# Kernel tuning notes

Measured on AMD Instinct MI355X. Metric: run time of the kernel, lower is better.

## Reference

```python
import jax, jax.numpy as jnp
import numpy as np

N = 48000      # total nodes
R = 16         # topological rounds
NPR = 3000     # nodes per round
DEG = 2        # children (incoming edges) per parent node
EPR = NPR * DEG
H = 128        # h_size
X = 128        # x_size
G = 16         # graphs in batch
PG = N // G    # nodes per graph == max_node_num


def setup_inputs() -> dict:
    key = jax.random.key(0)
    ks = jax.random.split(key, 8)
    j = np.arange(NPR)
    # round r parents are nodes [r*NPR,(r+1)*NPR); children come from round r-1
    edges = []
    for r in range(1, R):
        src = r * NPR + np.repeat(j, DEG)                                  # parent (edge_index[0])
        dst = (r - 1) * NPR + np.stack([j, (j + 1) % NPR], 1).ravel()       # child  (edge_index[1])
        edges.append(np.stack([src, dst], 0))
    edges_r = jnp.asarray(np.stack(edges, 0), dtype=jnp.int32)             # [R-1, 2, EPR]
    order_r = jnp.asarray(np.stack([r * NPR + j for r in range(1, R)], 0), dtype=jnp.int32)  # [R-1, NPR]
    order0 = jnp.asarray(j, dtype=jnp.int32)                               # leaves, round 0
    graph_idx = jnp.asarray(np.arange(N) // PG, dtype=jnp.int32)
    pos_idx = jnp.asarray(np.arange(N) % PG, dtype=jnp.int32)
    s = jnp.float32(0.05)
    return {
        'x': jax.random.normal(ks[0], (N, X), jnp.float32),
        'edge_labels_r': jax.random.randint(ks[1], (R - 1, EPR, 1), 0, 2).astype(jnp.float32),
        'W_iou': jax.random.normal(ks[2], (3 * H, X), jnp.float32) * s,
        'W_f': jax.random.normal(ks[3], (H, X), jnp.float32) * s,
        'b_iou': jax.random.normal(ks[4], (1, 3 * H), jnp.float32) * s,
        'b_f': jax.random.normal(ks[5], (1, H), jnp.float32) * s,
        'U_iou': jax.random.normal(ks[6], (3 * H, 2 * H), jnp.float32) * s,
        'U_f': jax.random.normal(ks[7], (H, 2 * H), jnp.float32) * s,
        'edges_r': edges_r,
        'order0': order0,
        'order_r': order_r,
        'graph_idx': graph_idx,
        'pos_idx': pos_idx,
        'graph_num': G,
        'max_node_num': PG,
    }


def reference(x, edge_labels_r, W_iou, W_f, b_iou, b_f, U_iou, U_f,
              edges_r, order0, order_r, graph_idx, pos_idx, graph_num, max_node_num):
    n = x.shape[0]
    h_size = W_f.shape[0]
    iou_x = x @ W_iou.T    # [n, 3h]
    wf_x = x @ W_f.T       # [n, h]

    def node_update(h, c, iou_mid, order):
        iou = iou_x[order] + iou_mid[order] + b_iou
        i, o, u = jnp.split(iou, 3, axis=1)
        c_temp = jax.nn.sigmoid(i) * jnp.tanh(u) + c[order]
        c = c.at[order].set(c_temp)
        h = h.at[order].set(jax.nn.sigmoid(o) * jnp.tanh(c_temp))
        return h, c

    h = jnp.zeros((n, h_size), x.dtype)
    c = jnp.zeros_like(h)
    iou_mid = jnp.zeros((n, 3 * h_size), x.dtype)
    h, c = node_update(h, c, iou_mid, order0)

    def step(carry, inp):
        h, c, iou_mid = carry
        edges, lab, order = inp        # edges [2,EPR], lab [EPR,1], order [NPR]
        src, child = edges[0], edges[1]
        h_j = h[child]
        # h_t0 (label==0 part) first, then h_t1, matching torch cat order
        h_two = jnp.concatenate([(1.0 - lab) * h_j, lab * h_j], axis=1)   # [EPR, 2h]
        iou_mid = iou_mid.at[src].add(h_two @ U_iou.T)
        f = jax.nn.sigmoid(wf_x[child] + h_two @ U_f.T + b_f)
        c = c.at[src].add(f * jnp.clip(c[child], -1e14, 1e14))
        h, c = node_update(h, c, iou_mid, order)
        return (h, c, iou_mid), None

    (h, c, iou_mid), _ = jax.lax.scan(step, (h, c, iou_mid), (edges_r, edge_labels_r, order_r))

    h_out = jnp.zeros((graph_num, max_node_num, h_size), x.dtype)
    return h_out.at[graph_idx, pos_idx].set(h)
```

## Files before the change

### kernel.cpp

```cpp
#include <hip/hip_runtime.h>
#include <math.h>

#define NN   48000
#define RR   16
#define NPR  3000
#define EPR  6000
#define HH   128
#define XX   128
#define C512 512

#define PPB  12
#define NB   250
#define MAXP 27
#define MAXE 52

typedef __attribute__((ext_vector_type(8))) short short8;
typedef __attribute__((ext_vector_type(8))) unsigned short ushort8;
typedef __attribute__((ext_vector_type(4))) float f32x4;

__device__ __forceinline__ float sigm(float v) {
  return __fdividef(1.0f, 1.0f + __expf(-v));
}
__device__ __forceinline__ float tanh_fast(float v) {
  return 1.0f - 2.0f * __fdividef(1.0f, 1.0f + __expf(2.0f * v));
}
__device__ __forceinline__ float clampc(float v) {
  return fminf(fmaxf(v, -1e14f), 1e14f);
}
__device__ __forceinline__ unsigned short f2bf(float f) {
  unsigned int u = __float_as_uint(f);
  unsigned int r = (u + 0x7FFFu + ((u >> 16) & 1u)) >> 16;
  return (unsigned short)r;
}

__global__ __launch_bounds__(256) void prep_wu(
    const float* __restrict__ Wiou, const float* __restrict__ Wf,
    const float* __restrict__ Uiou, const float* __restrict__ Uf,
    const float* __restrict__ b_iou, const float* __restrict__ b_f,
    unsigned short* __restrict__ Wbf, unsigned short* __restrict__ Ubf,
    float* __restrict__ biof) {
  int t = blockIdx.x * 256 + threadIdx.x;
  if (t < 512) biof[t] = (t < 384) ? b_iou[t] : b_f[t - 384];
  if (t < 512 * 128) {
    int r = t >> 7, c = t & 127;
    float v = (r < 384) ? Wiou[r * 128 + c] : Wf[(r - 384) * 128 + c];
    Wbf[t] = f2bf(v);
  }
  if (t < 512 * 256) {
    int r = t >> 8, c = t & 255;
    float v = (r < 384) ? Uiou[r * 256 + c] : Uf[(r - 384) * 256 + c];
    Ubf[t] = f2bf(v);
  }
}

__global__ __launch_bounds__(256) void pre_gemm_mfma(
    const float* __restrict__ x, const unsigned short* __restrict__ Wbf,
    const float* __restrict__ biof, float* __restrict__ pre) {
  __shared__ __align__(16) unsigned short A[128][136];
  const int n0 = blockIdx.x * 128;
  const int k0 = blockIdx.y * 128;
  const int t = threadIdx.x;

#pragma unroll
  for (int pass = 0; pass < 4; ++pass) {
    int row = (t >> 3) + pass * 32;
    int cb = (t & 7) * 16;
    const float* src = x + (size_t)(n0 + row) * XX + cb;
    unsigned short hv[16];
#pragma unroll
    for (int i = 0; i < 16; i += 4) {
      float4 v = *(const float4*)(src + i);
      hv[i] = f2bf(v.x); hv[i + 1] = f2bf(v.y);
      hv[i + 2] = f2bf(v.z); hv[i + 3] = f2bf(v.w);
    }
    *(ushort8*)&A[row][cb] = *(ushort8*)&hv[0];
    *(ushort8*)&A[row][cb + 8] = *(ushort8*)&hv[8];
  }
  __syncthreads();

  const int wave = t >> 6, lane = t & 63;
  const int wm = (wave & 1) * 64;
  const int wn = (wave >> 1) * 64;
  const int ln = lane & 15, q = lane >> 4;

  f32x4 acc[4][4];
#pragma unroll
  for (int mt = 0; mt < 4; ++mt)
#pragma unroll
    for (int nt = 0; nt < 4; ++nt)
      acc[mt][nt] = (f32x4){0.f, 0.f, 0.f, 0.f};

#pragma unroll
  for (int kt = 0; kt < 4; ++kt) {
    short8 af[4], bfr[4];
#pragma unroll
    for (int mt = 0; mt < 4; ++mt)
      af[mt] = *(const short8*)&A[wm + mt * 16 + ln][kt * 32 + q * 8];
#pragma unroll
    for (int nt = 0; nt < 4; ++nt)
      bfr[nt] = *(const short8*)(Wbf + (size_t)(k0 + wn + nt * 16 + ln) * 128 +
                                 kt * 32 + q * 8);
#pragma unroll
    for (int mt = 0; mt < 4; ++mt)
#pragma unroll
      for (int nt = 0; nt < 4; ++nt)
        acc[mt][nt] = __builtin_amdgcn_mfma_f32_16x16x32_bf16(
            af[mt], bfr[nt], acc[mt][nt], 0, 0, 0);
  }
  float bv[4];
#pragma unroll
  for (int nt = 0; nt < 4; ++nt) bv[nt] = biof[k0 + wn + nt * 16 + ln];
#pragma unroll
  for (int mt = 0; mt < 4; ++mt)
#pragma unroll
    for (int nt = 0; nt < 4; ++nt)
#pragma unroll
      for (int r = 0; r < 4; ++r)
        pre[(size_t)(n0 + wm + mt * 16 + q * 4 + r) * C512 +
            (k0 + wn + nt * 16 + ln)] = acc[mt][nt][r] + bv[nt];
}

__global__ __launch_bounds__(1024, 4) void rounds_halo(
    const float* __restrict__ pre, const unsigned short* __restrict__ Ubf,
    const float* __restrict__ labels, const int* __restrict__ order0,
    const int* __restrict__ order_r, float* __restrict__ hout) {
  __shared__ float Cp[2][MAXP + 1][132];
  __shared__ unsigned char labA[15 * 56];
  __shared__ int ordA[16 * 28];
  __shared__ __align__(16) unsigned short Abuf[56][264];
  __shared__ float Sb[26][392];
  __shared__ float Fb[52][132];

  const int t = threadIdx.x;
  const int b = blockIdx.x;
  const int g0 = b * PPB;
  const int w = t >> 6, lane = t & 63;
  const int ln = lane & 15, q = lane >> 4;

  if (t < 15 * 56) {
    int rr = t / 56, e = t - rr * 56;
    int p = e >> 1;
    int gp = g0 + p; if (gp >= NPR) gp -= NPR;
    labA[t] = (labels[(size_t)rr * EPR + 2 * gp + (e & 1)] >= 0.5f) ? 1 : 0;
  }
  if (t < 16 * 28) {
    int rr = t / 28, p = t - rr * 28;
    int gp = g0 + p; if (gp >= NPR) gp -= NPR;
    ordA[t] = (rr == 0) ? order0[gp] : order_r[(size_t)(rr - 1) * NPR + gp];
  }
  __syncthreads();

  const unsigned short* const ubase = Ubf + (size_t)(w * 32 + ln) * 256 + q * 8;

#pragma unroll
  for (int i = 0; i < 4; ++i) {
    int idx = t + i * 1024;
    int row = idx >> 7, j = idx & 127;
    if (row < MAXP) {
      int n = ordA[row];
      const float* pr = pre + (size_t)n * C512;
      float ct = sigm(pr[j]) * tanh_fast(pr[256 + j]);
      float ht = sigm(pr[128 + j]) * tanh_fast(ct);
      Cp[0][row][j] = ct;
      unsigned short hb = f2bf(ht);
      int L0 = labA[2 * row];
      Abuf[2 * row][j + (L0 ? 128 : 0)] = hb;
      Abuf[2 * row][j + (L0 ? 0 : 128)] = 0;
      if (row >= 1) {
        int L1 = labA[2 * row - 1];
        Abuf[2 * row - 1][j + (L1 ? 128 : 0)] = hb;
        Abuf[2 * row - 1][j + (L1 ? 0 : 128)] = 0;
      }
      if (row < PPB) hout[(size_t)n * HH + j] = ht;
    }
  }

  for (int r = 1; r < RR; ++r) {
    const int prv = (r - 1) & 1, cur = r & 1;
    const int Pr = MAXP - r;
    const int Er = 2 * Pr;
    const int NT = (Er + 15) >> 4;
    const int NIv = (Pr + 7) >> 3;

    __syncthreads();

    f32x4 acc[4][2];
#pragma unroll
    for (int mt = 0; mt < 4; ++mt)
#pragma unroll
      for (int nt = 0; nt < 2; ++nt)
        acc[mt][nt] = (f32x4){0.f, 0.f, 0.f, 0.f};

    short8 cb0 = *(const short8*)(ubase);
    short8 cb1 = *(const short8*)(ubase + (size_t)(16 * 256));
#pragma unroll
    for (int kt = 0; kt < 8; ++kt) {
      short8 nb0 = cb0, nb1 = cb1;
      if (kt < 7) {
        nb0 = *(const short8*)(ubase + (size_t)(kt + 1) * 32);
        nb1 = *(const short8*)(ubase + (size_t)(16 * 256) + (kt + 1) * 32);
      }
#pragma unroll
      for (int mt = 0; mt < 4; ++mt) {
        if (mt < NT) {
          short8 af = *(const short8*)&Abuf[mt * 16 + ln][kt * 32 + q * 8];
          acc[mt][0] = __builtin_amdgcn_mfma_f32_16x16x32_bf16(
              af, cb0, acc[mt][0], 0, 0, 0);
          acc[mt][1] = __builtin_amdgcn_mfma_f32_16x16x32_bf16(
              af, cb1, acc[mt][1], 0, 0, 0);
        }
      }
      cb0 = nb0; cb1 = nb1;
    }

#pragma unroll
    for (int mt = 0; mt < 4; ++mt) {
      if (mt < NT) {
#pragma unroll
        for (int nt = 0; nt < 2; ++nt) {
          int colg = w * 32 + nt * 16 + ln;
          if (colg < 384) {
#pragma unroll
            for (int rs = 0; rs < 2; ++rs) {
              int prow = mt * 8 + q * 2 + rs;
              if (prow < Pr)
                Sb[prow][colg] = acc[mt][nt][2 * rs] + acc[mt][nt][2 * rs + 1];
            }
          } else {
#pragma unroll
            for (int rr2 = 0; rr2 < 4; ++rr2) {
              int erow = mt * 16 + q * 4 + rr2;
              if (erow < Er) Fb[erow][colg - 384] = acc[mt][nt][rr2];
            }
          }
        }
      }
    }
    __syncthreads();

#pragma unroll
    for (int i = 0; i < 4; ++i) {
      if (i < NIv) {
        int idx = t + i * 1024;
        int p = idx >> 7, j = idx & 127;
        if (p < Pr) {
          int n  = ordA[r * 28 + p];
          int n0 = ordA[(r - 1) * 28 + p];
          int n1 = ordA[(r - 1) * 28 + p + 1];
          const float* pr = pre + (size_t)n * C512;
          float gi = pr[j] + Sb[p][j];
          float go = pr[128 + j] + Sb[p][128 + j];
          float gu = pr[256 + j] + Sb[p][256 + j];
          float wf0 = pre[(size_t)n0 * C512 + 384 + j];
          float wf1 = pre[(size_t)n1 * C512 + 384 + j];
          float f0 = sigm(wf0 + Fb[2 * p][j]);
          float f1 = sigm(wf1 + Fb[2 * p + 1][j]);
          float facc = f0 * clampc(Cp[prv][p][j]) +
                       f1 * clampc(Cp[prv][p + 1][j]);
          float ct = sigm(gi) * tanh_fast(gu) + facc;
          float ht = sigm(go) * tanh_fast(ct);
          Cp[cur][p][j] = ct;
          unsigned short hb = f2bf(ht);
          if (r < RR - 1) {
            int L0 = labA[r * 56 + 2 * p];
            Abuf[2 * p][j + (L0 ? 128 : 0)] = hb;
            Abuf[2 * p][j + (L0 ? 0 : 128)] = 0;
            if (p >= 1) {
              int L1 = labA[r * 56 + 2 * p - 1];
              Abuf[2 * p - 1][j + (L1 ? 128 : 0)] = hb;
              Abuf[2 * p - 1][j + (L1 ? 0 : 128)] = 0;
            }
          }
          if (p < PPB) hout[(size_t)n * HH + j] = ht;
        }
      }
    }
  }
}

extern "C" void kernel_launch(void* const* d_in, const int* in_sizes, int n_in,
                              void* d_out, int out_size, void* d_ws, size_t ws_size,
                              hipStream_t stream) {
  const float* x       = (const float*)d_in[0];
  const float* labels  = (const float*)d_in[1];
  const float* Wiou    = (const float*)d_in[2];
  const float* Wf      = (const float*)d_in[3];
  const float* b_iou   = (const float*)d_in[4];
  const float* b_f     = (const float*)d_in[5];
  const float* Uiou    = (const float*)d_in[6];
  const float* Uf      = (const float*)d_in[7];
  const int*   order0  = (const int*)d_in[9];
  const int*   order_r = (const int*)d_in[10];

  float* hout = (float*)d_out;

  float* pre  = (float*)d_ws;
  unsigned short* Wbf = (unsigned short*)(pre + (size_t)NN * C512);
  unsigned short* Ubf = Wbf + 512 * 128;
  float* biof = (float*)(Ubf + 512 * 256);

  prep_wu<<<512, 256, 0, stream>>>(Wiou, Wf, Uiou, Uf, b_iou, b_f,
                                   Wbf, Ubf, biof);
  pre_gemm_mfma<<<dim3(NN / 128, C512 / 128), 256, 0, stream>>>(x, Wbf, biof,
                                                                pre);
  rounds_halo<<<NB, 1024, 0, stream>>>(pre, Ubf, labels, order0, order_r,
                                       hout);
}
```

Measured before the change: 316.6 us.

## Fuse input projection GEMM into per-round recurrent kernel, drop pre buffer

Removes the separate x@W GEMM that wrote a 48000x512 fp32 pre-activation buffer to global memory. Instead x is converted to bf16 once, and each round of the recurrent kernel computes the input projection for its halo nodes with MFMA, staging results in shared memory (forget-gate part as bf16 in a double buffer). The aim is to cut global memory traffic and one kernel launch, at the cost of recomputing halo rows across blocks, an extra barrier per round, and more shared memory per block.

```diff
diff --git a/kernel.cpp b/kernel.cpp
--- a/kernel.cpp
+++ b/kernel.cpp
@@ -7,12 +7,10 @@
 #define EPR  6000
 #define HH   128
 #define XX   128
-#define C512 512
 
 #define PPB  12
 #define NB   250
 #define MAXP 27
-#define MAXE 52
 
 typedef __attribute__((ext_vector_type(8))) short short8;
 typedef __attribute__((ext_vector_type(8))) unsigned short ushort8;
@@ -32,15 +30,17 @@
   unsigned int r = (u + 0x7FFFu + ((u >> 16) & 1u)) >> 16;
   return (unsigned short)r;
 }
-
-__global__ __launch_bounds__(256) void prep_wu(
+__device__ __forceinline__ float bf2f(unsigned short h) {
+  return __uint_as_float(((unsigned int)h) << 16);
+}
+
+__global__ __launch_bounds__(256) void prep_wux(
     const float* __restrict__ Wiou, const float* __restrict__ Wf,
     const float* __restrict__ Uiou, const float* __restrict__ Uf,
-    const float* __restrict__ b_iou, const float* __restrict__ b_f,
+    const float* __restrict__ x,
     unsigned short* __restrict__ Wbf, unsigned short* __restrict__ Ubf,
-    float* __restrict__ biof) {
+    unsigned short* __restrict__ xbf) {
   int t = blockIdx.x * 256 + threadIdx.x;
-  if (t < 512) biof[t] = (t < 384) ? b_iou[t] : b_f[t - 384];
   if (t < 512 * 128) {
     int r = t >> 7, c = t & 127;
     float v = (r < 384) ? Wiou[r * 128 + c] : Wf[(r - 384) * 128 + c];
@@ -51,85 +51,25 @@
     float v = (r < 384) ? Uiou[r * 256 + c] : Uf[(r - 384) * 256 + c];
     Ubf[t] = f2bf(v);
   }
-}
-
-__global__ __launch_bounds__(256) void pre_gemm_mfma(
-    const float* __restrict__ x, const unsigned short* __restrict__ Wbf,
-    const float* __restrict__ biof, float* __restrict__ pre) {
-  __shared__ __align__(16) unsigned short A[128][136];
-  const int n0 = blockIdx.x * 128;
-  const int k0 = blockIdx.y * 128;
-  const int t = threadIdx.x;
-
-#pragma unroll
-  for (int pass = 0; pass < 4; ++pass) {
-    int row = (t >> 3) + pass * 32;
-    int cb = (t & 7) * 16;
-    const float* src = x + (size_t)(n0 + row) * XX + cb;
-    unsigned short hv[16];
-#pragma unroll
-    for (int i = 0; i < 16; i += 4) {
-      float4 v = *(const float4*)(src + i);
-      hv[i] = f2bf(v.x); hv[i + 1] = f2bf(v.y);
-      hv[i + 2] = f2bf(v.z); hv[i + 3] = f2bf(v.w);
-    }
-    *(ushort8*)&A[row][cb] = *(ushort8*)&hv[0];
-    *(ushort8*)&A[row][cb + 8] = *(ushort8*)&hv[8];
-  }
-  __syncthreads();
-
-  const int wave = t >> 6, lane = t & 63;
-  const int wm = (wave & 1) * 64;
-  const int wn = (wave >> 1) * 64;
-  const int ln = lane & 15, q = lane >> 4;
-
-  f32x4 acc[4][4];
-#pragma unroll
-  for (int mt = 0; mt < 4; ++mt)
-#pragma unroll
-    for (int nt = 0; nt < 4; ++nt)
-      acc[mt][nt] = (f32x4){0.f, 0.f, 0.f, 0.f};
-
-#pragma unroll
-  for (int kt = 0; kt < 4; ++kt) {
-    short8 af[4], bfr[4];
-#pragma unroll
-    for (int mt = 0; mt < 4; ++mt)
-      af[mt] = *(const short8*)&A[wm + mt * 16 + ln][kt * 32 + q * 8];
-#pragma unroll
-    for (int nt = 0; nt < 4; ++nt)
-      bfr[nt] = *(const short8*)(Wbf + (size_t)(k0 + wn + nt * 16 + ln) * 128 +
-                                 kt * 32 + q * 8);
-#pragma unroll
-    for (int mt = 0; mt < 4; ++mt)
-#pragma unroll
-      for (int nt = 0; nt < 4; ++nt)
-        acc[mt][nt] = __builtin_amdgcn_mfma_f32_16x16x32_bf16(
-            af[mt], bfr[nt], acc[mt][nt], 0, 0, 0);
-  }
-  float bv[4];
-#pragma unroll
-  for (int nt = 0; nt < 4; ++nt) bv[nt] = biof[k0 + wn + nt * 16 + ln];
-#pragma unroll
-  for (int mt = 0; mt < 4; ++mt)
-#pragma unroll
-    for (int nt = 0; nt < 4; ++nt)
-#pragma unroll
-      for (int r = 0; r < 4; ++r)
-        pre[(size_t)(n0 + wm + mt * 16 + q * 4 + r) * C512 +
-            (k0 + wn + nt * 16 + ln)] = acc[mt][nt][r] + bv[nt];
-}
-
-__global__ __launch_bounds__(1024, 4) void rounds_halo(
-    const float* __restrict__ pre, const unsigned short* __restrict__ Ubf,
+  for (int i = t; i < NN * XX; i += 3072 * 256) xbf[i] = f2bf(x[i]);
+}
+
+__global__ __launch_bounds__(1024, 4) void rounds_fused(
+    const unsigned short* __restrict__ xbf,
+    const unsigned short* __restrict__ Wbf,
+    const unsigned short* __restrict__ Ubf,
     const float* __restrict__ labels, const int* __restrict__ order0,
-    const int* __restrict__ order_r, float* __restrict__ hout) {
+    const int* __restrict__ order_r,
+    const float* __restrict__ b_iou, const float* __restrict__ b_f,
+    float* __restrict__ hout) {
   __shared__ float Cp[2][MAXP + 1][132];
+  __shared__ float bio[512];
   __shared__ unsigned char labA[15 * 56];
   __shared__ int ordA[16 * 28];
-  __shared__ __align__(16) unsigned short Abuf[56][264];
-  __shared__ float Sb[26][392];
+  __shared__ __align__(16) unsigned short Abuf[64][264];
+  __shared__ float Sb[27][394];
   __shared__ float Fb[52][132];
+  __shared__ unsigned short FwB[2][MAXP + 1][136];
 
   const int t = threadIdx.x;
   const int b = blockIdx.x;
@@ -137,6 +77,7 @@
   const int w = t >> 6, lane = t & 63;
   const int ln = lane & 15, q = lane >> 4;
 
+  if (t < 512) bio[t] = (t < 384) ? b_iou[t] : b_f[t - 384];
   if (t < 15 * 56) {
     int rr = t / 56, e = t - rr * 56;
     int p = e >> 1;
@@ -148,30 +89,71 @@
     int gp = g0 + p; if (gp >= NPR) gp -= NPR;
     ordA[t] = (rr == 0) ? order0[gp] : order_r[(size_t)(rr - 1) * NPR + gp];
   }
+  for (int i = t; i < 16 * 264; i += 1024)
+    Abuf[48 + i / 264][i % 264] = 0;
   __syncthreads();
 
   const unsigned short* const ubase = Ubf + (size_t)(w * 32 + ln) * 256 + q * 8;
-
-#pragma unroll
-  for (int i = 0; i < 4; ++i) {
-    int idx = t + i * 1024;
-    int row = idx >> 7, j = idx & 127;
-    if (row < MAXP) {
-      int n = ordA[row];
-      const float* pr = pre + (size_t)n * C512;
-      float ct = sigm(pr[j]) * tanh_fast(pr[256 + j]);
-      float ht = sigm(pr[128 + j]) * tanh_fast(ct);
-      Cp[0][row][j] = ct;
-      unsigned short hb = f2bf(ht);
-      int L0 = labA[2 * row];
-      Abuf[2 * row][j + (L0 ? 128 : 0)] = hb;
-      Abuf[2 * row][j + (L0 ? 0 : 128)] = 0;
-      if (row >= 1) {
-        int L1 = labA[2 * row - 1];
-        Abuf[2 * row - 1][j + (L1 ? 128 : 0)] = hb;
-        Abuf[2 * row - 1][j + (L1 ? 0 : 128)] = 0;
-      }
-      if (row < PPB) hout[(size_t)n * HH + j] = ht;
+  const unsigned short* const wbase = Wbf + (size_t)(w * 32 + ln) * 128 + q * 8;
+
+  {
+    int c1 = 16 + ln; if (c1 > 27) c1 = 27;
+    int rid0 = ordA[ln];
+    int rid1 = ordA[c1];
+    f32x4 accX[2][2];
+#pragma unroll
+    for (int mt = 0; mt < 2; ++mt)
+#pragma unroll
+      for (int nt = 0; nt < 2; ++nt)
+        accX[mt][nt] = (f32x4){0.f, 0.f, 0.f, 0.f};
+#pragma unroll
+    for (int kt = 0; kt < 4; ++kt) {
+      short8 ax0 = *(const short8*)(xbf + (size_t)rid0 * 128 + kt * 32 + q * 8);
+      short8 ax1 = *(const short8*)(xbf + (size_t)rid1 * 128 + kt * 32 + q * 8);
+      short8 bw0 = *(const short8*)(wbase + (size_t)kt * 32);
+      short8 bw1 = *(const short8*)(wbase + (size_t)(16 * 128) + kt * 32);
+      accX[0][0] = __builtin_amdgcn_mfma_f32_16x16x32_bf16(ax0, bw0, accX[0][0], 0, 0, 0);
+      accX[0][1] = __builtin_amdgcn_mfma_f32_16x16x32_bf16(ax0, bw1, accX[0][1], 0, 0, 0);
+      accX[1][0] = __builtin_amdgcn_mfma_f32_16x16x32_bf16(ax1, bw0, accX[1][0], 0, 0, 0);
+      accX[1][1] = __builtin_amdgcn_mfma_f32_16x16x32_bf16(ax1, bw1, accX[1][1], 0, 0, 0);
+    }
+#pragma unroll
+    for (int mt = 0; mt < 2; ++mt)
+#pragma unroll
+      for (int nt = 0; nt < 2; ++nt) {
+        int colg = w * 32 + nt * 16 + ln;
+#pragma unroll
+        for (int reg = 0; reg < 4; ++reg) {
+          int p = mt * 16 + q * 4 + reg;
+          if (p < MAXP) {
+            if (colg < 384) Sb[p][colg] = accX[mt][nt][reg];
+            else FwB[0][p][colg - 384] = f2bf(accX[mt][nt][reg]);
+          }
+        }
+      }
+    __syncthreads();
+#pragma unroll
+    for (int i = 0; i < 4; ++i) {
+      int idx = t + i * 1024;
+      int p = idx >> 7, j = idx & 127;
+      if (p < MAXP) {
+        float gi = Sb[p][j] + bio[j];
+        float go = Sb[p][128 + j] + bio[128 + j];
+        float gu = Sb[p][256 + j] + bio[256 + j];
+        float ct = sigm(gi) * tanh_fast(gu);
+        float ht = sigm(go) * tanh_fast(ct);
+        Cp[0][p][j] = ct;
+        unsigned short hb = f2bf(ht);
+        int L0 = labA[2 * p];
+        Abuf[2 * p][j + (L0 ? 128 : 0)] = hb;
+        Abuf[2 * p][j + (L0 ? 0 : 128)] = 0;
+        if (p >= 1) {
+          int L1 = labA[2 * p - 1];
+          Abuf[2 * p - 1][j + (L1 ? 128 : 0)] = hb;
+          Abuf[2 * p - 1][j + (L1 ? 0 : 128)] = 0;
+        }
+        if (p < PPB) hout[(size_t)ordA[p] * HH + j] = ht;
+      }
     }
   }
 
@@ -184,12 +166,49 @@
 
     __syncthreads();
 
-    f32x4 acc[4][2];
+    {
+      int c1 = 16 + ln; if (c1 > 27) c1 = 27;
+      int rid0 = ordA[r * 28 + ln];
+      int rid1 = ordA[r * 28 + c1];
+      f32x4 accX[2][2];
+#pragma unroll
+      for (int mt = 0; mt < 2; ++mt)
+#pragma unroll
+        for (int nt = 0; nt < 2; ++nt)
+          accX[mt][nt] = (f32x4){0.f, 0.f, 0.f, 0.f};
+#pragma unroll
+      for (int kt = 0; kt < 4; ++kt) {
+        short8 ax0 = *(const short8*)(xbf + (size_t)rid0 * 128 + kt * 32 + q * 8);
+        short8 ax1 = *(const short8*)(xbf + (size_t)rid1 * 128 + kt * 32 + q * 8);
+        short8 bw0 = *(const short8*)(wbase + (size_t)kt * 32);
+        short8 bw1 = *(const short8*)(wbase + (size_t)(16 * 128) + kt * 32);
+        accX[0][0] = __builtin_amdgcn_mfma_f32_16x16x32_bf16(ax0, bw0, accX[0][0], 0, 0, 0);
+        accX[0][1] = __builtin_amdgcn_mfma_f32_16x16x32_bf16(ax0, bw1, accX[0][1], 0, 0, 0);
+        accX[1][0] = __builtin_amdgcn_mfma_f32_16x16x32_bf16(ax1, bw0, accX[1][0], 0, 0, 0);
+        accX[1][1] = __builtin_amdgcn_mfma_f32_16x16x32_bf16(ax1, bw1, accX[1][1], 0, 0, 0);
+      }
+#pragma unroll
+      for (int mt = 0; mt < 2; ++mt)
+#pragma unroll
+        for (int nt = 0; nt < 2; ++nt) {
+          int colg = w * 32 + nt * 16 + ln;
+#pragma unroll
+          for (int reg = 0; reg < 4; ++reg) {
+            int p = mt * 16 + q * 4 + reg;
+            if (p < Pr) {
+              if (colg < 384) Sb[p][colg] = accX[mt][nt][reg];
+              else FwB[cur][p][colg - 384] = f2bf(accX[mt][nt][reg]);
+            }
+          }
+        }
+    }
+
+    f32x4 accU[4][2];
 #pragma unroll
     for (int mt = 0; mt < 4; ++mt)
 #pragma unroll
       for (int nt = 0; nt < 2; ++nt)
-        acc[mt][nt] = (f32x4){0.f, 0.f, 0.f, 0.f};
+        accU[mt][nt] = (f32x4){0.f, 0.f, 0.f, 0.f};
 
     short8 cb0 = *(const short8*)(ubase);
     short8 cb1 = *(const short8*)(ubase + (size_t)(16 * 256));
@@ -204,14 +223,15 @@
       for (int mt = 0; mt < 4; ++mt) {
         if (mt < NT) {
           short8 af = *(const short8*)&Abuf[mt * 16 + ln][kt * 32 + q * 8];
-          acc[mt][0] = __builtin_amdgcn_mfma_f32_16x16x32_bf16(
-              af, cb0, acc[mt][0], 0, 0, 0);
-          acc[mt][1] = __builtin_amdgcn_mfma_f32_16x16x32_bf16(
-              af, cb1, acc[mt][1], 0, 0, 0);
+          accU[mt][0] = __builtin_amdgcn_mfma_f32_16x16x32_bf16(
+              af, cb0, accU[mt][0], 0, 0, 0);
+          accU[mt][1] = __builtin_amdgcn_mfma_f32_16x16x32_bf16(
+              af, cb1, accU[mt][1], 0, 0, 0);
         }
       }
       cb0 = nb0; cb1 = nb1;
     }
+    __syncthreads();
 
 #pragma unroll
     for (int mt = 0; mt < 4; ++mt) {
@@ -224,13 +244,13 @@
             for (int rs = 0; rs < 2; ++rs) {
               int prow = mt * 8 + q * 2 + rs;
               if (prow < Pr)
-                Sb[prow][colg] = acc[mt][nt][2 * rs] + acc[mt][nt][2 * rs + 1];
+                Sb[prow][colg] += accU[mt][nt][2 * rs] + accU[mt][nt][2 * rs + 1];
             }
           } else {
 #pragma unroll
-            for (int rr2 = 0; rr2 < 4; ++rr2) {
-              int erow = mt * 16 + q * 4 + rr2;
-              if (erow < Er) Fb[erow][colg - 384] = acc[mt][nt][rr2];
+            for (int reg = 0; reg < 4; ++reg) {
+              int erow = mt * 16 + q * 4 + reg;
+              if (erow < Er) Fb[erow][colg - 384] = accU[mt][nt][reg];
             }
           }
         }
@@ -244,17 +264,13 @@
         int idx = t + i * 1024;
         int p = idx >> 7, j = idx & 127;
         if (p < Pr) {
-          int n  = ordA[r * 28 + p];
-          int n0 = ordA[(r - 1) * 28 + p];
-          int n1 = ordA[(r - 1) * 28 + p + 1];
-          const float* pr = pre + (size_t)n * C512;
-          float gi = pr[j] + Sb[p][j];
-          float go = pr[128 + j] + Sb[p][128 + j];
-          float gu = pr[256 + j] + Sb[p][256 + j];
-          float wf0 = pre[(size_t)n0 * C512 + 384 + j];
-          float wf1 = pre[(size_t)n1 * C512 + 384 + j];
-          float f0 = sigm(wf0 + Fb[2 * p][j]);
-          float f1 = sigm(wf1 + Fb[2 * p + 1][j]);
+          float gi = Sb[p][j] + bio[j];
+          float go = Sb[p][128 + j] + bio[128 + j];
+          float gu = Sb[p][256 + j] + bio[256 + j];
+          float wf0 = bf2f(FwB[prv][p][j]);
+          float wf1 = bf2f(FwB[prv][p + 1][j]);
+          float f0 = sigm(wf0 + Fb[2 * p][j] + bio[384 + j]);
+          float f1 = sigm(wf1 + Fb[2 * p + 1][j] + bio[384 + j]);
           float facc = f0 * clampc(Cp[prv][p][j]) +
                        f1 * clampc(Cp[prv][p + 1][j]);
           float ct = sigm(gi) * tanh_fast(gu) + facc;
@@ -271,7 +287,7 @@
               Abuf[2 * p - 1][j + (L1 ? 0 : 128)] = 0;
             }
           }
-          if (p < PPB) hout[(size_t)n * HH + j] = ht;
+          if (p < PPB) hout[(size_t)ordA[r * 28 + p] * HH + j] = ht;
         }
       }
     }
@@ -294,15 +310,11 @@
 
   float* hout = (float*)d_out;
 
-  float* pre  = (float*)d_ws;
-  unsigned short* Wbf = (unsigned short*)(pre + (size_t)NN * C512);
+  unsigned short* xbf = (unsigned short*)d_ws;
+  unsigned short* Wbf = xbf + (size_t)NN * XX;
   unsigned short* Ubf = Wbf + 512 * 128;
-  float* biof = (float*)(Ubf + 512 * 256);
-
-  prep_wu<<<512, 256, 0, stream>>>(Wiou, Wf, Uiou, Uf, b_iou, b_f,
-                                   Wbf, Ubf, biof);
-  pre_gemm_mfma<<<dim3(NN / 128, C512 / 128), 256, 0, stream>>>(x, Wbf, biof,
-                                                                pre);
-  rounds_halo<<<NB, 1024, 0, stream>>>(pre, Ubf, labels, order0, order_r,
-                                       hout);
-}
+
+  prep_wux<<<3072, 256, 0, stream>>>(Wiou, Wf, Uiou, Uf, x, Wbf, Ubf, xbf);
+  rounds_fused<<<NB, 1024, 0, stream>>>(xbf, Wbf, Ubf, labels, order0,
+                                        order_r, b_iou, b_f, hout);
+}
```

Measured after the change: 381.1 us. 20.4% more time.

## Load x tile once per block and loop over all output columns with transposed MFMA

Applied to the files above, without the earlier changes.

The pre-GEMM grid drops its column dimension, so each block converts its 128-row x tile to bf16 once and loops over all four 128-column output chunks. The MFMA operands are swapped (weights as A, x as B) so each lane's accumulator holds four consecutive output columns, which allows float4 stores of the pre buffer and float4 bias loads. This removes the redundant x reads and conversions across the former column blocks. In exchange it gives four times fewer blocks, each with a longer serial loop.

```diff
diff --git a/kernel.cpp b/kernel.cpp
--- a/kernel.cpp
+++ b/kernel.cpp
@@ -58,7 +58,6 @@
     const float* __restrict__ biof, float* __restrict__ pre) {
   __shared__ __align__(16) unsigned short A[128][136];
   const int n0 = blockIdx.x * 128;
-  const int k0 = blockIdx.y * 128;
   const int t = threadIdx.x;
 
 #pragma unroll
@@ -79,45 +78,51 @@
   __syncthreads();
 
   const int wave = t >> 6, lane = t & 63;
-  const int wm = (wave & 1) * 64;
+  const int wk = (wave & 1) * 64;
   const int wn = (wave >> 1) * 64;
   const int ln = lane & 15, q = lane >> 4;
 
-  f32x4 acc[4][4];
-#pragma unroll
-  for (int mt = 0; mt < 4; ++mt)
-#pragma unroll
-    for (int nt = 0; nt < 4; ++nt)
-      acc[mt][nt] = (f32x4){0.f, 0.f, 0.f, 0.f};
-
-#pragma unroll
-  for (int kt = 0; kt < 4; ++kt) {
-    short8 af[4], bfr[4];
+  for (int ko = 0; ko < 4; ++ko) {
+    const int k0 = ko * 128;
+    f32x4 acc[4][4];
 #pragma unroll
     for (int mt = 0; mt < 4; ++mt)
-      af[mt] = *(const short8*)&A[wm + mt * 16 + ln][kt * 32 + q * 8];
-#pragma unroll
-    for (int nt = 0; nt < 4; ++nt)
-      bfr[nt] = *(const short8*)(Wbf + (size_t)(k0 + wn + nt * 16 + ln) * 128 +
-                                 kt * 32 + q * 8);
-#pragma unroll
-    for (int mt = 0; mt < 4; ++mt)
 #pragma unroll
       for (int nt = 0; nt < 4; ++nt)
-        acc[mt][nt] = __builtin_amdgcn_mfma_f32_16x16x32_bf16(
-            af[mt], bfr[nt], acc[mt][nt], 0, 0, 0);
-  }
-  float bv[4];
-#pragma unroll
-  for (int nt = 0; nt < 4; ++nt) bv[nt] = biof[k0 + wn + nt * 16 + ln];
-#pragma unroll
-  for (int mt = 0; mt < 4; ++mt)
-#pragma unroll
-    for (int nt = 0; nt < 4; ++nt)
-#pragma unroll
-      for (int r = 0; r < 4; ++r)
-        pre[(size_t)(n0 + wm + mt * 16 + q * 4 + r) * C512 +
-            (k0 + wn + nt * 16 + ln)] = acc[mt][nt][r] + bv[nt];
+        acc[mt][nt] = (f32x4){0.f, 0.f, 0.f, 0.f};
+
+#pragma unroll
+    for (int kt = 0; kt < 4; ++kt) {
+      short8 af[4], bfr[4];
+#pragma unroll
+      for (int mt = 0; mt < 4; ++mt)
+        af[mt] = *(const short8*)(Wbf +
+            (size_t)(k0 + wk + mt * 16 + ln) * 128 + kt * 32 + q * 8);
+#pragma unroll
+      for (int nt = 0; nt < 4; ++nt)
+        bfr[nt] = *(const short8*)&A[wn + nt * 16 + ln][kt * 32 + q * 8];
+#pragma unroll
+      for (int mt = 0; mt < 4; ++mt)
+#pragma unroll
+        for (int nt = 0; nt < 4; ++nt)
+          acc[mt][nt] = __builtin_amdgcn_mfma_f32_16x16x32_bf16(
+              af[mt], bfr[nt], acc[mt][nt], 0, 0, 0);
+    }
+#pragma unroll
+    for (int mt = 0; mt < 4; ++mt) {
+      float4 bv = *(const float4*)(biof + k0 + wk + mt * 16 + q * 4);
+#pragma unroll
+      for (int nt = 0; nt < 4; ++nt) {
+        float4 o;
+        o.x = acc[mt][nt][0] + bv.x;
+        o.y = acc[mt][nt][1] + bv.y;
+        o.z = acc[mt][nt][2] + bv.z;
+        o.w = acc[mt][nt][3] + bv.w;
+        *(float4*)(pre + (size_t)(n0 + wn + nt * 16 + ln) * C512 +
+                   k0 + wk + mt * 16 + q * 4) = o;
+      }
+    }
+  }
 }
 
 __global__ __launch_bounds__(1024, 4) void rounds_halo(
@@ -301,8 +306,7 @@
 
   prep_wu<<<512, 256, 0, stream>>>(Wiou, Wf, Uiou, Uf, b_iou, b_f,
                                    Wbf, Ubf, biof);
-  pre_gemm_mfma<<<dim3(NN / 128, C512 / 128), 256, 0, stream>>>(x, Wbf, biof,
-                                                                pre);
+  pre_gemm_mfma<<<NN / 128, 256, 0, stream>>>(x, Wbf, biof, pre);
   rounds_halo<<<NB, 1024, 0, stream>>>(pre, Ubf, labels, order0, order_r,
                                        hout);
 }
```

Result: slower. 328.7 us (+3.8%).
